# Kernel tuning notes

Hardware: AMD Instinct MI355X
Metric: run time of the kernel (lower is better)

The kernel has to match this reference:

```python
import jax, jax.numpy as jnp
import numpy as np

B, C, H, W = 16, 256, 128, 128
K = 21                 # max kernel size: relu(.)*20 + 1 in [1, 21]
P = (K - 1) // 2       # reflect padding for max kernel


def setup_inputs() -> dict:
    key = jax.random.key(0)
    k0, k1, k2, k3 = jax.random.split(key, 4)
    x = jax.random.normal(k0, (B, C, H, W), jnp.float32)
    # depthwise Gaussian-like base kernel [C, 1, K, K]
    gauss_kernel = jax.random.uniform(k1, (C, 1, K, K), jnp.float32) * (1.0 / (K * K))
    # kernel-size predictor params (1x1 convs)
    w1 = jax.random.normal(k2, (32, C, 1, 1), jnp.float32) * 0.1
    b1 = jnp.zeros((32,), jnp.float32)
    w2 = jax.random.normal(k3, (1, 32, 1, 1), jnp.float32) * 0.1
    b2 = jnp.ones((1,), jnp.float32)
    return {"x": x, "gauss_kernel": gauss_kernel, "w1": w1, "b1": b1, "w2": w2, "b2": b2}


def reference(x, gauss_kernel, w1, b1, w2, b2):
    # KernelSizePredictor: 1x1 conv -> relu -> 1x1 conv, then relu(.)*20 + 1
    h = jax.nn.relu(jnp.einsum('bchw,oc->bohw', x, w1[:, :, 0, 0]) + b1[None, :, None, None])
    pred = jax.nn.relu(jnp.einsum('bohw,po->bphw', h, w2[:, :, 0, 0]) + b2[None, :, None, None]) * 20.0 + 1.0
    # per-sample scalar kernel size (int(kernel_sizes[i].item()) intent)
    ksz = jnp.clip(jnp.floor(jnp.mean(pred, axis=(1, 2, 3))), 1.0, float(K))   # [B]
    rad = jnp.floor((ksz - 1.0) / 2.0)                                          # [B]
    # mask fixed KxK kernel down to the per-sample adaptive size
    coords = jnp.abs(jnp.arange(K, dtype=x.dtype) - P)                          # [K]
    mask = ((coords[None, :, None] <= rad[:, None, None]) &
            (coords[None, None, :] <= rad[:, None, None])).astype(x.dtype)      # [B,K,K]
    kern = gauss_kernel[None] * mask[:, None, None]                              # [B,C,1,K,K]
    # reflect pad then per-sample depthwise conv (groups = C), VALID -> same HxW
    xp = jnp.pad(x, ((0, 0), (0, 0), (P, P), (P, P)), mode='reflect')

    def conv_one(xi, ki):
        return jax.lax.conv_general_dilated(
            xi[None], ki, window_strides=(1, 1), padding='VALID',
            feature_group_count=C,
            dimension_numbers=('NCHW', 'OIHW', 'NCHW'))[0]

    return jax.vmap(conv_one)(xp, kern)   # [B, C, H, W]
```

## Files before the change

kernel.cpp:

```cpp
#include <hip/hip_runtime.h>

#define HW 16384
#define CCH 256
#define XS_STRIDE 168
#define WM_STRIDE 22
#define WT_STRIDE 264

typedef _Float16 f16x8 __attribute__((ext_vector_type(8)));
typedef _Float16 f16x4 __attribute__((ext_vector_type(4)));
typedef float f32x4 __attribute__((ext_vector_type(4)));

__global__ __launch_bounds__(256) void pred_kernel(
    const float* __restrict__ x, const float* __restrict__ w1,
    const float* __restrict__ b1, const float* __restrict__ w2,
    const float* __restrict__ b2, float* __restrict__ sums) {
  __shared__ _Float16 wt[32 * WT_STRIDE];
  __shared__ _Float16 xt[64 * WT_STRIDE];
  __shared__ float wsum[4];

  const int tid = threadIdx.x;
  const int b = blockIdx.y;
  const int pix0 = blockIdx.x * 64;
  const float* xb = x + (size_t)b * CCH * HW + pix0;

  for (int i = tid; i < 32 * 256; i += 256) {
    int o = i >> 8, c = i & 255;
    wt[o * WT_STRIDE + c] = (_Float16)w1[i];
  }
  for (int it = 0; it < 16; ++it) {
    int flat = it * 1024 + tid * 4;
    int c = flat >> 6, px = flat & 63;
    float4 v = *(const float4*)(xb + (size_t)c * HW + px);
    xt[(px + 0) * WT_STRIDE + c] = (_Float16)v.x;
    xt[(px + 1) * WT_STRIDE + c] = (_Float16)v.y;
    xt[(px + 2) * WT_STRIDE + c] = (_Float16)v.z;
    xt[(px + 3) * WT_STRIDE + c] = (_Float16)v.w;
  }
  __syncthreads();

  const int lane = tid & 63;
  const int w = tid >> 6;
  const int n_l = lane & 15;
  const int q = lane >> 4;

  f32x4 acc0 = {0.f, 0.f, 0.f, 0.f};
  f32x4 acc1 = {0.f, 0.f, 0.f, 0.f};
  const _Float16* wrow0 = wt + n_l * WT_STRIDE;
  const _Float16* wrow1 = wt + (16 + n_l) * WT_STRIDE;
  const _Float16* xrow  = xt + (16 * w + n_l) * WT_STRIDE;

#pragma unroll
  for (int ck = 0; ck < 8; ++ck) {
    int co = ck * 32 + 8 * q;
    f16x8 Bv = *(const f16x8*)(xrow + co);
    f16x8 A0 = *(const f16x8*)(wrow0 + co);
    f16x8 A1 = *(const f16x8*)(wrow1 + co);
    acc0 = __builtin_amdgcn_mfma_f32_16x16x32_f16(A0, Bv, acc0, 0, 0, 0);
    acc1 = __builtin_amdgcn_mfma_f32_16x16x32_f16(A1, Bv, acc1, 0, 0, 0);
  }

  float zp = 0.f;
#pragma unroll
  for (int e = 0; e < 4; ++e) {
    int o0 = 4 * q + e, o1 = 16 + 4 * q + e;
    zp += fmaxf(acc0[e] + b1[o0], 0.f) * w2[o0];
    zp += fmaxf(acc1[e] + b1[o1], 0.f) * w2[o1];
  }
  zp += __shfl_xor(zp, 16);
  zp += __shfl_xor(zp, 32);
  float pred = (fmaxf(zp + b2[0], 0.f) * 20.f + 1.f) * 0.25f;
#pragma unroll
  for (int off = 32; off > 0; off >>= 1) pred += __shfl_down(pred, off);
  if (lane == 0) wsum[w] = pred;
  __syncthreads();
  if (tid == 0) atomicAdd(&sums[b], wsum[0] + wsum[1] + wsum[2] + wsum[3]);
}

__global__ void finalize_kernel(const float* __restrict__ sums,
                                int* __restrict__ rads) {
  int t = threadIdx.x;
  if (t < 16) {
    float mean = sums[t] * (1.f / (float)HW);
    float ksz = fminf(fmaxf(floorf(mean), 1.f), 21.f);
    rads[t] = (int)floorf((ksz - 1.f) * 0.5f);
  }
}

template <int CB, int CNT>
__device__ __forceinline__ void conv_chunk(const _Float16* xs, const _Float16* wm,
                                           f32x4 (&acc)[8], int lane, int wrow) {
  const int n_l = lane & 15;
  const int q = lane >> 4;
  const int kb = q * 8;

  f16x8 Bf[CNT];
#pragma unroll
  for (int d = 0; d < CNT; ++d) {
    f16x8 v;
#pragma unroll
    for (int j = 0; j < 8; ++j) {
      int t = kb + j - n_l;
      int tc = t < 0 ? 0 : (t > 20 ? 20 : t);
      _Float16 wv = wm[(CB + d) * WM_STRIDE + tc];
      v[j] = (t >= 0 && t <= 20) ? wv : (_Float16)0.f;
    }
    Bf[d] = v;
  }
  f16x8 B2f;
#pragma unroll
  for (int j = 0; j < 8; ++j) {
    int jj = kb + j;
    int d8 = jj >> 2, k2 = jj & 3;
    int dcl = d8 < CNT ? d8 : CNT - 1;
    int t = 32 + k2 - n_l;
    int tc = t > 20 ? 20 : t;
    _Float16 wv = wm[(CB + dcl) * WM_STRIDE + tc];
    B2f[j] = (t <= 20 && d8 < CNT) ? wv : (_Float16)0.f;
  }
  const int kya = CB + ((2 * q) < CNT ? 2 * q : CNT - 1);
  const int kyb = CB + ((2 * q + 1) < CNT ? 2 * q + 1 : CNT - 1);

#pragma unroll
  for (int tx = 0; tx < 8; ++tx) {
    f32x4 a = acc[tx];
    const _Float16* base = xs + (wrow + n_l) * XS_STRIDE + 16 * tx + kb;
#pragma unroll
    for (int d = 0; d < CNT; ++d) {
      f16x8 av = *(const f16x8*)(base + (CB + d) * XS_STRIDE);
      a = __builtin_amdgcn_mfma_f32_16x16x32_f16(av, Bf[d], a, 0, 0, 0);
    }
    {
      const _Float16* pa = xs + (wrow + kya + n_l) * XS_STRIDE + 16 * tx + 32;
      const _Float16* pb = xs + (wrow + kyb + n_l) * XS_STRIDE + 16 * tx + 32;
      f16x4 lo = *(const f16x4*)pa;
      f16x4 hi = *(const f16x4*)pb;
      f16x8 av;
      av[0] = lo[0]; av[1] = lo[1]; av[2] = lo[2]; av[3] = lo[3];
      av[4] = hi[0]; av[5] = hi[1]; av[6] = hi[2]; av[7] = hi[3];
      a = __builtin_amdgcn_mfma_f32_16x16x32_f16(av, B2f, a, 0, 0, 0);
    }
    acc[tx] = a;
  }
}

__global__ __launch_bounds__(256) void conv_kernel(
    const float* __restrict__ x, const float* __restrict__ gauss,
    const int* __restrict__ rads, float* __restrict__ out) {
  __shared__ _Float16 xs[84 * XS_STRIDE];
  __shared__ _Float16 wm[21 * WM_STRIDE];

  const int half = blockIdx.x;
  const int c = blockIdx.y, b = blockIdx.z;
  const int y0 = half * 64;
  const int tid = threadIdx.x;
  const int r = rads[b];
  const float* img = x + ((size_t)(b * CCH + c)) * HW;

  for (int i = tid; i < 84 * 148; i += 256) {
    int row = i / 148, col = i - row * 148;
    int gy = y0 + row - 10; gy = gy < 0 ? -gy : (gy > 127 ? 254 - gy : gy);
    int gx = col - 10;      gx = gx < 0 ? -gx : (gx > 127 ? 254 - gx : gx);
    xs[row * XS_STRIDE + col] = (_Float16)img[gy * 128 + gx];
  }
  for (int i = tid; i < 441; i += 256) {
    int ky = i / 21, kx = i - ky * 21;
    int ay = ky - 10; ay = ay < 0 ? -ay : ay;
    int ax = kx - 10; ax = ax < 0 ? -ax : ax;
    float wv = (ay <= r && ax <= r) ? gauss[(size_t)c * 441 + i] : 0.f;
    wm[ky * WM_STRIDE + kx] = (_Float16)wv;
  }
  __syncthreads();

  const int lane = tid & 63;
  const int w = tid >> 6;
  const int wrow = 16 * w;
  f32x4 acc[8];
#pragma unroll
  for (int j = 0; j < 8; ++j) {
    f32x4 z = {0.f, 0.f, 0.f, 0.f};
    acc[j] = z;
  }

  conv_chunk<0, 8>(xs, wm, acc, lane, wrow);
  conv_chunk<8, 8>(xs, wm, acc, lane, wrow);
  conv_chunk<16, 5>(xs, wm, acc, lane, wrow);

  float* outc = out + ((size_t)(b * CCH + c)) * HW;
  const int row0 = (lane >> 4) * 4;
  const int coln = lane & 15;
#pragma unroll
  for (int tx = 0; tx < 8; ++tx) {
    f32x4 a = acc[tx];
    float* po = outc + (size_t)(y0 + wrow + row0) * 128 + 16 * tx + coln;
#pragma unroll
    for (int e = 0; e < 4; ++e) po[e * 128] = a[e];
  }
}

extern "C" void kernel_launch(void* const* d_in, const int* in_sizes, int n_in,
                              void* d_out, int out_size, void* d_ws, size_t ws_size,
                              hipStream_t stream) {
  const float* x     = (const float*)d_in[0];
  const float* gauss = (const float*)d_in[1];
  const float* w1    = (const float*)d_in[2];
  const float* b1    = (const float*)d_in[3];
  const float* w2    = (const float*)d_in[4];
  const float* b2    = (const float*)d_in[5];
  float* out = (float*)d_out;

  float* sums = (float*)d_ws;
  int* rads = (int*)((char*)d_ws + 64);

  (void)hipMemsetAsync(d_ws, 0, 64, stream);
  pred_kernel<<<dim3(256, 16), 256, 0, stream>>>(x, w1, b1, w2, b2, sums);
  finalize_kernel<<<1, 64, 0, stream>>>(sums, rads);
  conv_kernel<<<dim3(2, 256, 16), 256, 0, stream>>>(x, gauss, rads, out);
}
```

Baseline: 646.2 us.

## Swizzle conv LDS tile, chunk predictor over channels, fold finalize into conv

The predictor kernel now handles 256 pixels per block and streams channels in 32-channel chunks through a channel-major LDS buffer, which cuts the block count and avoids the transposed scalar LDS stores. The conv kernel stores its input tile with an XOR swizzle and vectorized 8-wide f16 writes to reduce LDS bank conflicts, and it sets a launch-bounds occupancy hint. The finalize kernel is removed and each conv block computes the radius from the sums directly, which saves one launch. The risks are more barriers inside the predictor loop and higher LDS use per conv block from the wider stride.

Result: faster. 631.5 us (-2.3%).

```diff
diff --git a/kernel.cpp b/kernel.cpp
--- a/kernel.cpp
+++ b/kernel.cpp
@@ -2,12 +2,14 @@
 
 #define HW 16384
 #define CCH 256
-#define XS_STRIDE 168
+#define XS_STRIDE 192
 #define WM_STRIDE 22
 #define WT_STRIDE 264
+#define PS 258
 
 typedef _Float16 f16x8 __attribute__((ext_vector_type(8)));
 typedef _Float16 f16x4 __attribute__((ext_vector_type(4)));
+typedef _Float16 f16x2 __attribute__((ext_vector_type(2)));
 typedef float f32x4 __attribute__((ext_vector_type(4)));
 
 __global__ __launch_bounds__(256) void pred_kernel(
@@ -15,76 +17,78 @@
     const float* __restrict__ b1, const float* __restrict__ w2,
     const float* __restrict__ b2, float* __restrict__ sums) {
   __shared__ _Float16 wt[32 * WT_STRIDE];
-  __shared__ _Float16 xt[64 * WT_STRIDE];
+  __shared__ _Float16 xc[32 * PS];
   __shared__ float wsum[4];
 
   const int tid = threadIdx.x;
   const int b = blockIdx.y;
-  const int pix0 = blockIdx.x * 64;
-  const float* xb = x + (size_t)b * CCH * HW + pix0;
-
-  for (int i = tid; i < 32 * 256; i += 256) {
-    int o = i >> 8, c = i & 255;
-    wt[o * WT_STRIDE + c] = (_Float16)w1[i];
-  }
-  for (int it = 0; it < 16; ++it) {
-    int flat = it * 1024 + tid * 4;
-    int c = flat >> 6, px = flat & 63;
-    float4 v = *(const float4*)(xb + (size_t)c * HW + px);
-    xt[(px + 0) * WT_STRIDE + c] = (_Float16)v.x;
-    xt[(px + 1) * WT_STRIDE + c] = (_Float16)v.y;
-    xt[(px + 2) * WT_STRIDE + c] = (_Float16)v.z;
-    xt[(px + 3) * WT_STRIDE + c] = (_Float16)v.w;
-  }
-  __syncthreads();
+  const int px0 = blockIdx.x * 256;
+  const float* xb = x + (size_t)b * CCH * HW + px0;
+
+  for (int i = tid; i < 32 * 256; i += 256)
+    wt[(i >> 8) * WT_STRIDE + (i & 255)] = (_Float16)w1[i];
 
   const int lane = tid & 63;
   const int w = tid >> 6;
   const int n_l = lane & 15;
   const int q = lane >> 4;
 
-  f32x4 acc0 = {0.f, 0.f, 0.f, 0.f};
-  f32x4 acc1 = {0.f, 0.f, 0.f, 0.f};
-  const _Float16* wrow0 = wt + n_l * WT_STRIDE;
-  const _Float16* wrow1 = wt + (16 + n_l) * WT_STRIDE;
-  const _Float16* xrow  = xt + (16 * w + n_l) * WT_STRIDE;
-
-#pragma unroll
+  f32x4 acc0[4], acc1[4];
+#pragma unroll
+  for (int i = 0; i < 4; ++i) {
+    f32x4 z = {0.f, 0.f, 0.f, 0.f};
+    acc0[i] = z; acc1[i] = z;
+  }
+
   for (int ck = 0; ck < 8; ++ck) {
-    int co = ck * 32 + 8 * q;
-    f16x8 Bv = *(const f16x8*)(xrow + co);
-    f16x8 A0 = *(const f16x8*)(wrow0 + co);
-    f16x8 A1 = *(const f16x8*)(wrow1 + co);
-    acc0 = __builtin_amdgcn_mfma_f32_16x16x32_f16(A0, Bv, acc0, 0, 0, 0);
-    acc1 = __builtin_amdgcn_mfma_f32_16x16x32_f16(A1, Bv, acc1, 0, 0, 0);
-  }
-
-  float zp = 0.f;
-#pragma unroll
-  for (int e = 0; e < 4; ++e) {
-    int o0 = 4 * q + e, o1 = 16 + 4 * q + e;
-    zp += fmaxf(acc0[e] + b1[o0], 0.f) * w2[o0];
-    zp += fmaxf(acc1[e] + b1[o1], 0.f) * w2[o1];
-  }
-  zp += __shfl_xor(zp, 16);
-  zp += __shfl_xor(zp, 32);
-  float pred = (fmaxf(zp + b2[0], 0.f) * 20.f + 1.f) * 0.25f;
-#pragma unroll
-  for (int off = 32; off > 0; off >>= 1) pred += __shfl_down(pred, off);
-  if (lane == 0) wsum[w] = pred;
+    __syncthreads();
+#pragma unroll
+    for (int it = 0; it < 8; ++it) {
+      int flat = it * 1024 + tid * 4;
+      int cl = flat >> 8, px = flat & 255;
+      float4 v = *(const float4*)(xb + (size_t)(32 * ck + cl) * HW + px);
+      f16x2 p0 = {(_Float16)v.x, (_Float16)v.y};
+      f16x2 p1 = {(_Float16)v.z, (_Float16)v.w};
+      *(f16x2*)(&xc[cl * PS + px]) = p0;
+      *(f16x2*)(&xc[cl * PS + px + 2]) = p1;
+    }
+    __syncthreads();
+
+    f16x8 A0 = *(const f16x8*)(wt + n_l * WT_STRIDE + 32 * ck + 8 * q);
+    f16x8 A1 = *(const f16x8*)(wt + (16 + n_l) * WT_STRIDE + 32 * ck + 8 * q);
+#pragma unroll
+    for (int i = 0; i < 4; ++i) {
+      int pxb = 16 * (4 * i + w) + n_l;
+      f16x8 Bv;
+#pragma unroll
+      for (int j = 0; j < 8; ++j) Bv[j] = xc[(8 * q + j) * PS + pxb];
+      acc0[i] = __builtin_amdgcn_mfma_f32_16x16x32_f16(A0, Bv, acc0[i], 0, 0, 0);
+      acc1[i] = __builtin_amdgcn_mfma_f32_16x16x32_f16(A1, Bv, acc1[i], 0, 0, 0);
+    }
+  }
+
+  float psum = 0.f;
+#pragma unroll
+  for (int i = 0; i < 4; ++i) {
+    float zp = 0.f;
+#pragma unroll
+    for (int e = 0; e < 4; ++e) {
+      int o0 = 4 * q + e, o1 = 16 + 4 * q + e;
+      zp += fmaxf(acc0[i][e] + b1[o0], 0.f) * w2[o0];
+      zp += fmaxf(acc1[i][e] + b1[o1], 0.f) * w2[o1];
+    }
+    zp += __shfl_xor(zp, 16);
+    zp += __shfl_xor(zp, 32);
+    psum += fmaxf(zp + b2[0], 0.f) * 20.f + 1.f;
+  }
+#pragma unroll
+  for (int off = 32; off > 0; off >>= 1) psum += __shfl_down(psum, off);
+  if (lane == 0) wsum[w] = psum * 0.25f;
   __syncthreads();
   if (tid == 0) atomicAdd(&sums[b], wsum[0] + wsum[1] + wsum[2] + wsum[3]);
 }
 
-__global__ void finalize_kernel(const float* __restrict__ sums,
-                                int* __restrict__ rads) {
-  int t = threadIdx.x;
-  if (t < 16) {
-    float mean = sums[t] * (1.f / (float)HW);
-    float ksz = fminf(fmaxf(floorf(mean), 1.f), 21.f);
-    rads[t] = (int)floorf((ksz - 1.f) * 0.5f);
-  }
-}
+#define SWZ(row, col) ((row) * XS_STRIDE + ((col) ^ (((row) & 7) << 3)))
 
 template <int CB, int CNT>
 __device__ __forceinline__ void conv_chunk(const _Float16* xs, const _Float16* wm,
@@ -123,17 +127,16 @@
 #pragma unroll
   for (int tx = 0; tx < 8; ++tx) {
     f32x4 a = acc[tx];
-    const _Float16* base = xs + (wrow + n_l) * XS_STRIDE + 16 * tx + kb;
 #pragma unroll
     for (int d = 0; d < CNT; ++d) {
-      f16x8 av = *(const f16x8*)(base + (CB + d) * XS_STRIDE);
+      int row = wrow + n_l + CB + d;
+      f16x8 av = *(const f16x8*)(xs + SWZ(row, 16 * tx + kb));
       a = __builtin_amdgcn_mfma_f32_16x16x32_f16(av, Bf[d], a, 0, 0, 0);
     }
     {
-      const _Float16* pa = xs + (wrow + kya + n_l) * XS_STRIDE + 16 * tx + 32;
-      const _Float16* pb = xs + (wrow + kyb + n_l) * XS_STRIDE + 16 * tx + 32;
-      f16x4 lo = *(const f16x4*)pa;
-      f16x4 hi = *(const f16x4*)pb;
+      int ra = wrow + kya + n_l, rb = wrow + kyb + n_l;
+      f16x4 lo = *(const f16x4*)(xs + SWZ(ra, 16 * tx + 32));
+      f16x4 hi = *(const f16x4*)(xs + SWZ(rb, 16 * tx + 32));
       f16x8 av;
       av[0] = lo[0]; av[1] = lo[1]; av[2] = lo[2]; av[3] = lo[3];
       av[4] = hi[0]; av[5] = hi[1]; av[6] = hi[2]; av[7] = hi[3];
@@ -143,9 +146,9 @@
   }
 }
 
-__global__ __launch_bounds__(256) void conv_kernel(
+__global__ __launch_bounds__(256, 4) void conv_kernel(
     const float* __restrict__ x, const float* __restrict__ gauss,
-    const int* __restrict__ rads, float* __restrict__ out) {
+    const float* __restrict__ sums, float* __restrict__ out) {
   __shared__ _Float16 xs[84 * XS_STRIDE];
   __shared__ _Float16 wm[21 * WM_STRIDE];
 
@@ -153,14 +156,24 @@
   const int c = blockIdx.y, b = blockIdx.z;
   const int y0 = half * 64;
   const int tid = threadIdx.x;
-  const int r = rads[b];
+
+  float mean = sums[b] * (1.f / (float)HW);
+  float ksz = fminf(fmaxf(floorf(mean), 1.f), 21.f);
+  const int r = (int)floorf((ksz - 1.f) * 0.5f);
+
   const float* img = x + ((size_t)(b * CCH + c)) * HW;
 
-  for (int i = tid; i < 84 * 148; i += 256) {
-    int row = i / 148, col = i - row * 148;
+  for (int g = tid; g < 84 * 19; g += 256) {
+    int row = g / 19, cg = (g - row * 19) * 8;
     int gy = y0 + row - 10; gy = gy < 0 ? -gy : (gy > 127 ? 254 - gy : gy);
-    int gx = col - 10;      gx = gx < 0 ? -gx : (gx > 127 ? 254 - gx : gx);
-    xs[row * XS_STRIDE + col] = (_Float16)img[gy * 128 + gx];
+    const float* grow = img + gy * 128;
+    f16x8 v;
+#pragma unroll
+    for (int e = 0; e < 8; ++e) {
+      int gx = cg + e - 10; gx = gx < 0 ? -gx : (gx > 127 ? 254 - gx : gx);
+      v[e] = (_Float16)grow[gx];
+    }
+    *(f16x8*)(&xs[SWZ(row, cg)]) = v;
   }
   for (int i = tid; i < 441; i += 256) {
     int ky = i / 21, kx = i - ky * 21;
@@ -209,10 +222,8 @@
   float* out = (float*)d_out;
 
   float* sums = (float*)d_ws;
-  int* rads = (int*)((char*)d_ws + 64);
 
   (void)hipMemsetAsync(d_ws, 0, 64, stream);
-  pred_kernel<<<dim3(256, 16), 256, 0, stream>>>(x, w1, b1, w2, b2, sums);
-  finalize_kernel<<<1, 64, 0, stream>>>(sums, rads);
-  conv_kernel<<<dim3(2, 256, 16), 256, 0, stream>>>(x, gauss, rads, out);
-}
+  pred_kernel<<<dim3(64, 16), 256, 0, stream>>>(x, w1, b1, w2, b2, sums);
+  conv_kernel<<<dim3(2, 256, 16), 256, 0, stream>>>(x, gauss, sums, out);
+}
```
